# Optimization experiments

Hardware: AMD Instinct MI355X
Metric: run time of the kernel (lower is better)

## Reference

```python
import jax, jax.numpy as jnp
import numpy as np

H = 16          # bit depth; n = 2**H
K = 4           # f*H // division_fact = 2*16//8
TP = 8          # number of coordinate copies
N = 1 << H
T1 = 128        # query block
T2 = 512        # key block
D = 256         # euclidean embedding dim
C = 2 * K * H + 1  # connection candidates = 129


def _distance(c1, c2, norm):
    # sign/exponent 'critical graph' distance:
    # sg = sign(c1)*sign(c2); s = frexp_exponent(|c1|^|c2| + 1)/H
    sg = ((2 * (c1 >= 0).astype(jnp.int32) - 1) *
          (2 * (c2 >= 0).astype(jnp.int32) - 1)).astype(jnp.float32)
    xr = jnp.abs(c1) ^ jnp.abs(c2)
    _, e = jnp.frexp((xr + 1).astype(jnp.float32))
    return sg * (1.0 - e.astype(jnp.float32) / H) * norm


def setup_inputs() -> dict:
    key = jax.random.key(0)
    k1, k2, k3, k4, k5, k6 = jax.random.split(key, 6)
    emb_T1 = jax.random.normal(k1, (T1, D), jnp.float32)
    emb_T2 = jax.random.normal(k2, (T2, D), jnp.float32)
    # locations are signed integers in [1-n, n) as in __init__
    sta_loc = jax.random.randint(k3, (T1, TP), 1 - N, N, jnp.int32)
    pos_loc = jax.random.randint(k4, (T2, TP), 1 - N, N, jnp.int32)
    # neighbor valid_mask: choosing_mask = rand > 0.2
    mask = jax.random.bernoulli(k5, 0.8, (T1, T2))
    # raw random numbers for generate_random_masks (low-bit masks applied inside reference)
    random_masks = jax.random.randint(k6, (T1, H, K, TP), 0, N, jnp.int32)
    return {"emb_T1": emb_T1, "emb_T2": emb_T2, "sta_loc": sta_loc,
            "pos_loc": pos_loc, "mask": mask, "random_masks": random_masks}


def reference(emb_T1, emb_T2, sta_loc, pos_loc, mask, random_masks):
    # ---- connection(): bit-flip XOR candidate generation ----
    flip = (jnp.int32(1) << jnp.arange(H, dtype=jnp.int32))          # (H,)
    flipped = sta_loc[:, None, :] ^ flip[None, :, None]              # (T1, H, TP)
    low = random_masks & (flip - 1)[None, :, None, None]             # keep low i bits
    res = (flipped[:, :, None, :] ^ low).reshape(T1, H * K, TP)      # (T1, H*K, TP)
    cnc_loc = jnp.concatenate([res, sta_loc[:, None, :], -res], axis=1)  # (T1, C, TP)

    # ---- normalized_matmul -> target similarity val_v; val_n = ones ----
    e1 = emb_T1 / jnp.linalg.norm(emb_T1, axis=-1, keepdims=True)
    e2 = emb_T2 / jnp.linalg.norm(emb_T2, axis=-1, keepdims=True)
    val_v = e1 @ e2.T                                                # (T1, T2)

    # ---- distances (val_n == 1) ----
    dis_sta = _distance(sta_loc[:, None, :], pos_loc[None, :, :], 1.0)       # (T1,T2,TP)
    dsum = dis_sta.sum(-1)                                                   # (T1,T2)
    dis_cnc = _distance(cnc_loc[:, None, :, :], pos_loc[None, :, None, :], 1.0)  # (T1,T2,C,TP)
    ct_val = (dsum[:, :, None, None] - dis_sta[:, :, None, :] + dis_cnc) / TP    # (T1,T2,C,TP)

    # ---- masked MSE loss, summed over the T2 (neighbor) dim ----
    diff = ct_val - val_v[:, :, None, None]
    loss = (diff * diff * mask[:, :, None, None].astype(jnp.float32)).sum(axis=1)  # (T1,C,TP)
    return loss
```

## Files before the change

kernel.cpp:

```cpp
#include <hip/hip_runtime.h>
#include <stdint.h>

#define T1c 128
#define T2c 512
#define TPc 8
#define Cc  129
#define Dc  256
#define T2H 256
#define MBS 260

__device__ __forceinline__ int pack_loc(int v) {
    int a = v < 0 ? -v : v;
    return a | (v < 0 ? (int)0x80000000 : 0);
}

__device__ __forceinline__ void dist_core(unsigned v1, unsigned v2, float& dd, float& val) {
    unsigned xv = v1 ^ v2;
    unsigned xr = xv & 0x7FFFFFFFu;
    val = fmaf((float)__clz((int)(xr + 1u)), 0.0625f, -1.0f);
    dd  = __uint_as_float(__float_as_uint(val) ^ (xv & 0x80000000u));
}

__device__ __forceinline__ float wave_sum(float v) {
    #pragma unroll
    for (int off = 32; off; off >>= 1) v += __shfl_xor(v, off, 64);
    return v;
}

__global__ __launch_bounds__(512) void k_fused(
    const float* __restrict__ e1, const float* __restrict__ e2,
    const int* __restrict__ sta, const int* __restrict__ pos,
    const void* __restrict__ mask, const int* __restrict__ rm,
    float* __restrict__ out) {
    int b  = blockIdx.x;
    int t1 = b >> 1;
    int th = b & 1;
    int base = th * T2H;
    int tid  = threadIdx.x;
    int lane = tid & 63, wv = tid >> 6;

    __shared__ float se1[Dc];
    __shared__ float smb[TPc][MBS];
    __shared__ int   spp[TPc][MBS];
    __shared__ float smf[T2H];
    __shared__ float sred[4][9];
    __shared__ float sA[9];
    __shared__ float sdot[512], sss[512];
    __shared__ float sinv1;
    __shared__ int   sflag;

    if (tid == 0) sflag = 0;
    __syncthreads();
    if (((const unsigned char*)mask)[1 + 4 * tid] != 0) atomicOr(&sflag, 1);
    if (wv == 0) {
        float4 a = ((const float4*)(e1 + (size_t)t1 * Dc))[lane];
        ((float4*)se1)[lane] = a;
        float s = wave_sum(a.x * a.x + a.y * a.y + a.z * a.z + a.w * a.w);
        if (lane == 0) sinv1 = rsqrtf(s);
    }
    __syncthreads();

    {
        int t2l = tid >> 1, h = tid & 1;
        int t2  = base + t2l;
        const float4* xrow = (const float4*)(e2 + (size_t)t2 * Dc) + h * 32;
        const float4* arow = (const float4*)se1 + h * 32;
        float dot = 0.f, ss = 0.f;
        #pragma unroll 8
        for (int d = 0; d < 32; ++d) {
            float4 x = xrow[d];
            float4 a = arow[d];
            dot = fmaf(a.x, x.x, fmaf(a.y, x.y, fmaf(a.z, x.z, fmaf(a.w, x.w, dot))));
            ss  = fmaf(x.x, x.x, fmaf(x.y, x.y, fmaf(x.z, x.z, fmaf(x.w, x.w, ss))));
        }
        sdot[tid] = dot;
        sss[tid]  = ss;
    }
    __syncthreads();

    if (tid < T2H) {
        int t2 = base + tid;
        float dot = sdot[2 * tid] + sdot[2 * tid + 1];
        float ss  = sss[2 * tid]  + sss[2 * tid + 1];
        float vv  = dot * sinv1 * rsqrtf(ss);
        int idx = t1 * T2c + t2;
        float m;
        if (sflag) m = (((const unsigned char*)mask)[idx] != 0) ? 1.0f : 0.0f;
        else       m = (((const int*)mask)[idx] != 0) ? 1.0f : 0.0f;
        smf[tid] = m;

        int4 p0 = ((const int4*)(pos + (size_t)t2 * TPc))[0];
        int4 p1 = ((const int4*)(pos + (size_t)t2 * TPc))[1];
        int pk[8] = {pack_loc(p0.x), pack_loc(p0.y), pack_loc(p0.z), pack_loc(p0.w),
                     pack_loc(p1.x), pack_loc(p1.y), pack_loc(p1.z), pack_loc(p1.w)};
        int4 s0 = ((const int4*)(sta + (size_t)t1 * TPc))[0];
        int4 s1 = ((const int4*)(sta + (size_t)t1 * TPc))[1];
        int sk[8] = {pack_loc(s0.x), pack_loc(s0.y), pack_loc(s0.z), pack_loc(s0.w),
                     pack_loc(s1.x), pack_loc(s1.y), pack_loc(s1.z), pack_loc(s1.w)};
        float d[8];
        float dsum = 0.f;
        #pragma unroll
        for (int p = 0; p < 8; ++p) {
            float dd, val;
            dist_core((unsigned)sk[p], (unsigned)pk[p], dd, val);
            d[p] = dd;
            dsum += dd;
        }
        float acc[9];
        #pragma unroll
        for (int p = 0; p < 8; ++p) {
            float mb = m * ((dsum - d[p]) * 0.125f - vv);
            smb[p][tid] = mb;
            spp[p][tid] = pk[p];
            acc[p] = mb * mb;
        }
        float c6 = dsum * 0.125f - vv;
        acc[8] = m * c6 * c6;
        #pragma unroll
        for (int j = 0; j < 9; ++j) acc[j] = wave_sum(acc[j]);
        if (lane == 0) {
            #pragma unroll
            for (int j = 0; j < 9; ++j) sred[wv][j] = acc[j];
        }
    }
    __syncthreads();
    if (tid < 9) {
        float v = (sred[0][tid] + sred[1][tid]) + (sred[2][tid] + sred[3][tid]);
        sA[tid] = v;
    }
    __syncthreads();

    int p = tid & 7;
    int c = tid >> 3;
    int i = c >> 2, kk = c & 3;
    int stav = sta[t1 * TPc + p];
    int low  = rm[(((t1 * 16 + i) * 4 + kk) * TPc) + p] & ((1 << i) - 1);
    int resv = (stav ^ (1 << i)) ^ low;
    unsigned v1 = (unsigned)pack_loc(resv);

    const int4*   pp4 = (const int4*)&spp[p][0];
    const float4* mb4 = (const float4*)&smb[p][0];
    const float4* mf4 = (const float4*)smf;

    float B = 0.f, Q = 0.f;
    #pragma unroll 4
    for (int j = 0; j < 64; ++j) {
        int4   pv = pp4[j];
        float4 mb = mb4[j];
        float4 mm = mf4[j];
        float dd, val;
        dist_core(v1, (unsigned)pv.x, dd, val);
        B = fmaf(mb.x, dd, B); Q = fmaf(mm.x * val, val, Q);
        dist_core(v1, (unsigned)pv.y, dd, val);
        B = fmaf(mb.y, dd, B); Q = fmaf(mm.y * val, val, Q);
        dist_core(v1, (unsigned)pv.z, dd, val);
        B = fmaf(mb.z, dd, B); Q = fmaf(mm.z * val, val, Q);
        dist_core(v1, (unsigned)pv.w, dd, val);
        B = fmaf(mb.w, dd, B); Q = fmaf(mm.w * val, val, Q);
    }
    float A = sA[p];
    float core = fmaf(Q, 1.0f / 64.0f, A);
    float l0 = fmaf(B,  0.25f, core);
    float l1 = (resv == 0) ? l0 : fmaf(B, -0.25f, core);
    atomicAdd(&out[((size_t)t1 * Cc + c) * TPc + p], l0);
    atomicAdd(&out[((size_t)t1 * Cc + 65 + c) * TPc + p], l1);
    if (tid < 8) atomicAdd(&out[((size_t)t1 * Cc + 64) * TPc + tid], sA[8]);
}

extern "C" void kernel_launch(void* const* d_in, const int* in_sizes, int n_in,
                              void* d_out, int out_size, void* d_ws, size_t ws_size,
                              hipStream_t stream) {
    const float* emb1 = (const float*)d_in[0];
    const float* emb2 = (const float*)d_in[1];
    const int*   sta  = (const int*)d_in[2];
    const int*   pos  = (const int*)d_in[3];
    const void*  mask = d_in[4];
    const int*   rm   = (const int*)d_in[5];

    hipMemsetAsync(d_out, 0, (size_t)T1c * Cc * TPc * sizeof(float), stream);
    hipLaunchKernelGGL(k_fused, dim3(256), dim3(512), 0, stream,
                       emb1, emb2, sta, pos, mask, rm, (float*)d_out);
}
```

Measured before the change: 84.32 us.

## Split fused kernel into prep and main kernels via workspace, drop atomics

```diff
diff --git a/kernel.cpp b/kernel.cpp
--- a/kernel.cpp
+++ b/kernel.cpp
@@ -6,8 +6,13 @@
 #define TPc 8
 #define Cc  129
 #define Dc  256
-#define T2H 256
-#define MBS 260
+#define QT  128
+
+#define WS_MB   0
+#define WS_MF   524288
+#define WS_PP   589824
+#define WS_PA   593920
+#define WS_C64  598016
 
 __device__ __forceinline__ int pack_loc(int v) {
     int a = v < 0 ? -v : v;
@@ -16,8 +21,7 @@
 
 __device__ __forceinline__ void dist_core(unsigned v1, unsigned v2, float& dd, float& val) {
     unsigned xv = v1 ^ v2;
-    unsigned xr = xv & 0x7FFFFFFFu;
-    val = fmaf((float)__clz((int)(xr + 1u)), 0.0625f, -1.0f);
+    val = fmaf((float)__clz((int)((xv & 0x7FFFFFFFu) + 1u)), 0.0625f, -1.0f);
     dd  = __uint_as_float(__float_as_uint(val) ^ (xv & 0x80000000u));
 }
 
@@ -27,58 +31,55 @@
     return v;
 }
 
-__global__ __launch_bounds__(512) void k_fused(
+__global__ __launch_bounds__(256, 2) void k1_prep(
     const float* __restrict__ e1, const float* __restrict__ e2,
     const int* __restrict__ sta, const int* __restrict__ pos,
-    const void* __restrict__ mask, const int* __restrict__ rm,
-    float* __restrict__ out) {
+    const void* __restrict__ mask, float* __restrict__ ws) {
     int b  = blockIdx.x;
-    int t1 = b >> 1;
-    int th = b & 1;
-    int base = th * T2H;
+    int t1 = b >> 2;
+    int q  = b & 3;
+    int base = q * QT;
     int tid  = threadIdx.x;
     int lane = tid & 63, wv = tid >> 6;
 
     __shared__ float se1[Dc];
-    __shared__ float smb[TPc][MBS];
-    __shared__ int   spp[TPc][MBS];
-    __shared__ float smf[T2H];
-    __shared__ float sred[4][9];
-    __shared__ float sA[9];
-    __shared__ float sdot[512], sss[512];
+    __shared__ float sdot[256], sss[256];
+    __shared__ float sred[2][9];
     __shared__ float sinv1;
     __shared__ int   sflag;
 
     if (tid == 0) sflag = 0;
     __syncthreads();
     if (((const unsigned char*)mask)[1 + 4 * tid] != 0) atomicOr(&sflag, 1);
-    if (wv == 0) {
-        float4 a = ((const float4*)(e1 + (size_t)t1 * Dc))[lane];
-        ((float4*)se1)[lane] = a;
+    if (tid < 64) {
+        float4 a = ((const float4*)(e1 + (size_t)t1 * Dc))[tid];
+        ((float4*)se1)[tid] = a;
         float s = wave_sum(a.x * a.x + a.y * a.y + a.z * a.z + a.w * a.w);
-        if (lane == 0) sinv1 = rsqrtf(s);
+        if (tid == 0) sinv1 = rsqrtf(s);
     }
     __syncthreads();
 
     {
-        int t2l = tid >> 1, h = tid & 1;
-        int t2  = base + t2l;
+        int t2 = base + (tid >> 1), h = tid & 1;
         const float4* xrow = (const float4*)(e2 + (size_t)t2 * Dc) + h * 32;
         const float4* arow = (const float4*)se1 + h * 32;
-        float dot = 0.f, ss = 0.f;
+        float dx = 0.f, dy = 0.f, dz = 0.f, dw = 0.f;
+        float sx = 0.f, sy = 0.f, sz = 0.f, sw = 0.f;
         #pragma unroll 8
         for (int d = 0; d < 32; ++d) {
             float4 x = xrow[d];
             float4 a = arow[d];
-            dot = fmaf(a.x, x.x, fmaf(a.y, x.y, fmaf(a.z, x.z, fmaf(a.w, x.w, dot))));
-            ss  = fmaf(x.x, x.x, fmaf(x.y, x.y, fmaf(x.z, x.z, fmaf(x.w, x.w, ss))));
-        }
-        sdot[tid] = dot;
-        sss[tid]  = ss;
-    }
-    __syncthreads();
-
-    if (tid < T2H) {
+            dx = fmaf(a.x, x.x, dx); dy = fmaf(a.y, x.y, dy);
+            dz = fmaf(a.z, x.z, dz); dw = fmaf(a.w, x.w, dw);
+            sx = fmaf(x.x, x.x, sx); sy = fmaf(x.y, x.y, sy);
+            sz = fmaf(x.z, x.z, sz); sw = fmaf(x.w, x.w, sw);
+        }
+        sdot[tid] = (dx + dy) + (dz + dw);
+        sss[tid]  = (sx + sy) + (sz + sw);
+    }
+    __syncthreads();
+
+    if (tid < QT) {
         int t2 = base + tid;
         float dot = sdot[2 * tid] + sdot[2 * tid + 1];
         float ss  = sss[2 * tid]  + sss[2 * tid + 1];
@@ -87,7 +88,7 @@
         float m;
         if (sflag) m = (((const unsigned char*)mask)[idx] != 0) ? 1.0f : 0.0f;
         else       m = (((const int*)mask)[idx] != 0) ? 1.0f : 0.0f;
-        smf[tid] = m;
+        ws[WS_MF + idx] = m;
 
         int4 p0 = ((const int4*)(pos + (size_t)t2 * TPc))[0];
         int4 p1 = ((const int4*)(pos + (size_t)t2 * TPc))[1];
@@ -110,12 +111,16 @@
         #pragma unroll
         for (int p = 0; p < 8; ++p) {
             float mb = m * ((dsum - d[p]) * 0.125f - vv);
-            smb[p][tid] = mb;
-            spp[p][tid] = pk[p];
+            ws[WS_MB + ((size_t)t1 * TPc + p) * T2c + t2] = mb;
             acc[p] = mb * mb;
         }
         float c6 = dsum * 0.125f - vv;
         acc[8] = m * c6 * c6;
+        if (t1 == 0) {
+            int* wspp = (int*)(ws + WS_PP);
+            #pragma unroll
+            for (int p = 0; p < 8; ++p) wspp[p * T2c + t2] = pk[p];
+        }
         #pragma unroll
         for (int j = 0; j < 9; ++j) acc[j] = wave_sum(acc[j]);
         if (lane == 0) {
@@ -124,23 +129,33 @@
         }
     }
     __syncthreads();
-    if (tid < 9) {
-        float v = (sred[0][tid] + sred[1][tid]) + (sred[2][tid] + sred[3][tid]);
-        sA[tid] = v;
-    }
-    __syncthreads();
-
-    int p = tid & 7;
-    int c = tid >> 3;
-    int i = c >> 2, kk = c & 3;
+    if (tid < 8)  ws[WS_PA + (size_t)(t1 * 4 + q) * 8 + tid] = sred[0][tid] + sred[1][tid];
+    if (tid == 8) ws[WS_C64 + (size_t)(t1 * 4 + q)] = sred[0][8] + sred[1][8];
+}
+
+__global__ __launch_bounds__(256, 2) void k2_main(
+    const int* __restrict__ sta, const int* __restrict__ rm,
+    const float* __restrict__ ws, float* __restrict__ out) {
+    int b  = blockIdx.x;
+    int t1 = b >> 2;
+    int cg = b & 3;
+    int tid = threadIdx.x;
+    int p  = tid & 7;
+    int cl = (tid >> 3) & 15;
+    int h  = tid >> 7;
+    int c  = cg * 16 + cl;
+    int i  = c >> 2, kk = c & 3;
+
+    __shared__ float sB[256], sQ[256];
+
     int stav = sta[t1 * TPc + p];
     int low  = rm[(((t1 * 16 + i) * 4 + kk) * TPc) + p] & ((1 << i) - 1);
     int resv = (stav ^ (1 << i)) ^ low;
     unsigned v1 = (unsigned)pack_loc(resv);
 
-    const int4*   pp4 = (const int4*)&spp[p][0];
-    const float4* mb4 = (const float4*)&smb[p][0];
-    const float4* mf4 = (const float4*)smf;
+    const int4*   pp4 = (const int4*)((const int*)(ws + WS_PP) + p * T2c + h * 256);
+    const float4* mb4 = (const float4*)(ws + WS_MB + ((size_t)t1 * TPc + p) * T2c + h * 256);
+    const float4* mf4 = (const float4*)(ws + WS_MF + (size_t)t1 * T2c + h * 256);
 
     float B = 0.f, Q = 0.f;
     #pragma unroll 4
@@ -158,13 +173,25 @@
         dist_core(v1, (unsigned)pv.w, dd, val);
         B = fmaf(mb.w, dd, B); Q = fmaf(mm.w * val, val, Q);
     }
-    float A = sA[p];
-    float core = fmaf(Q, 1.0f / 64.0f, A);
-    float l0 = fmaf(B,  0.25f, core);
-    float l1 = (resv == 0) ? l0 : fmaf(B, -0.25f, core);
-    atomicAdd(&out[((size_t)t1 * Cc + c) * TPc + p], l0);
-    atomicAdd(&out[((size_t)t1 * Cc + 65 + c) * TPc + p], l1);
-    if (tid < 8) atomicAdd(&out[((size_t)t1 * Cc + 64) * TPc + tid], sA[8]);
+    sB[tid] = B;
+    sQ[tid] = Q;
+    __syncthreads();
+    if (h == 0) {
+        float Bs = B + sB[tid + 128];
+        float Qs = Q + sQ[tid + 128];
+        const float* PA = ws + WS_PA + (size_t)t1 * 32;
+        float A = (PA[p] + PA[8 + p]) + (PA[16 + p] + PA[24 + p]);
+        float core = fmaf(Qs, 1.0f / 64.0f, A);
+        float l0 = fmaf(Bs,  0.25f, core);
+        float l1 = (resv == 0) ? l0 : fmaf(Bs, -0.25f, core);
+        float* o = out + (size_t)t1 * Cc * TPc;
+        o[c * TPc + p]        = l0;
+        o[(65 + c) * TPc + p] = l1;
+        if (cg == 0 && tid < 8) {
+            const float* pc = ws + WS_C64 + (size_t)t1 * 4;
+            o[64 * TPc + tid] = (pc[0] + pc[1]) + (pc[2] + pc[3]);
+        }
+    }
 }
 
 extern "C" void kernel_launch(void* const* d_in, const int* in_sizes, int n_in,
@@ -177,7 +204,8 @@
     const void*  mask = d_in[4];
     const int*   rm   = (const int*)d_in[5];
 
-    hipMemsetAsync(d_out, 0, (size_t)T1c * Cc * TPc * sizeof(float), stream);
-    hipLaunchKernelGGL(k_fused, dim3(256), dim3(512), 0, stream,
-                       emb1, emb2, sta, pos, mask, rm, (float*)d_out);
-}
+    hipLaunchKernelGGL(k1_prep, dim3(512), dim3(256), 0, stream,
+                       emb1, emb2, sta, pos, mask, (float*)d_ws);
+    hipLaunchKernelGGL(k2_main, dim3(512), dim3(256), 0, stream,
+                       sta, rm, (const float*)d_ws, (float*)d_out);
+}
```

New measurement: 108.1 us. 1.28x slower.
